# Performance work log

Hardware: AMD Instinct MI355X
Metric: run time of the kernel (lower is better)

Reference implementation:

```python
import jax, jax.numpy as jnp
import numpy as np

N_NODES = 50000
N_EDGES = 800000
D_N = 64      # node feature dim
D_E = 64      # edge feature dim
HID = 128     # MLP hidden dim
D_OUT = 64    # edge/node MLP output dim


def _mlp_params(key, d_in, d_hid, d_out):
    k1, k2 = jax.random.split(key)
    s1 = 1.0 / np.sqrt(d_in)
    s2 = 1.0 / np.sqrt(d_hid)
    return (
        jax.random.uniform(k1, (d_in, d_hid), jnp.float32, -s1, s1),
        jnp.zeros((d_hid,), jnp.float32),
        jax.random.uniform(k2, (d_hid, d_out), jnp.float32, -s2, s2),
        jnp.zeros((d_out,), jnp.float32),
    )


def setup_inputs() -> dict:
    key = jax.random.key(0)
    ks = jax.random.split(key, 7)
    nf = jax.random.normal(ks[0], (N_NODES, D_N), jnp.float32)
    ef = jax.random.normal(ks[1], (N_EDGES, D_E), jnp.float32)
    src = jax.random.randint(ks[2], (N_EDGES,), 0, N_NODES, jnp.int64)
    dst = jax.random.randint(ks[3], (N_EDGES,), 0, N_NODES, jnp.int64)
    We1, be1, We2, be2 = _mlp_params(ks[4], 2 * D_N + D_E, HID, D_OUT)
    Wa1, ba1, Wa2, ba2 = _mlp_params(ks[5], 2 * D_N + D_E, HID, D_OUT)
    Wn1, bn1, Wn2, bn2 = _mlp_params(ks[6], D_OUT + D_N, HID, D_OUT)
    return dict(nf=nf, ef=ef, src=src, dst=dst,
                We1=We1, be1=be1, We2=We2, be2=be2,
                Wa1=Wa1, ba1=ba1, Wa2=Wa2, ba2=ba2,
                Wn1=Wn1, bn1=bn1, Wn2=Wn2, bn2=bn2)


def _mlp(x, W1, b1, W2, b2):
    return jax.nn.relu(x @ W1 + b1) @ W2 + b2


def reference(nf, ef, src, dst,
              We1, be1, We2, be2,
              Wa1, ba1, Wa2, ba2,
              Wn1, bn1, Wn2, bn2):
    # edge update: gather src/dst node feats, concat with edge feats  [E, 2*D_N + D_E]
    x_e = jnp.concatenate([nf[src], nf[dst], ef], axis=-1)
    e_out = _mlp(x_e, We1, be1, We2, be2)                 # [E, D_OUT]
    gate = jax.nn.sigmoid(_mlp(x_e, Wa1, ba1, Wa2, ba2))  # [E, D_OUT]
    updated_ef = gate * e_out                              # message m == updated edge feat
    # scatter-sum messages into destination nodes
    agg_m = jax.ops.segment_sum(updated_ef, dst, num_segments=N_NODES)  # [N, D_OUT]
    # node update
    x_n = jnp.concatenate([agg_m, nf], axis=-1)            # [N, D_OUT + D_N]
    updated_nf = _mlp(x_n, Wn1, bn1, Wn2, bn2)             # [N, D_OUT]
    return updated_nf, updated_ef
```

## Files before the change

kernel.cpp:

```cpp
#include <hip/hip_runtime.h>

#define NN 50000
#define NE 800000

typedef float f32x4 __attribute__((ext_vector_type(4)));
typedef short s16x8 __attribute__((ext_vector_type(8)));
typedef unsigned short u16;

__device__ __forceinline__ u16 f2bf(float f) {
  union { float f; unsigned u; } v; v.f = f;
  unsigned r = v.u + 0x7FFFu + ((v.u >> 16) & 1u);
  return (u16)(r >> 16);
}

__device__ __forceinline__ void st_bf4(u16* p, f32x4 v) {
  ushort4 pv;
  pv.x = f2bf(v.x); pv.y = f2bf(v.y); pv.z = f2bf(v.z); pv.w = f2bf(v.w);
  *(ushort4*)p = pv;
}

__global__ void zero_kernel(f32x4* __restrict__ p) {
  f32x4 z; z[0] = 0.f; z[1] = 0.f; z[2] = 0.f; z[3] = 0.f;
  p[(size_t)blockIdx.x * 256 + threadIdx.x] = z;
}

__device__ __forceinline__ void pack_one(const float* __restrict__ W, int N,
                                         u16* __restrict__ out, int t) {
  int j = t & 7, lane = (t >> 3) & 63, f = t >> 9;
  int NT = N >> 4;
  int nt = f % NT, ks = f / NT;
  int row = ks * 32 + ((lane >> 4) << 3) + j;
  int col = nt * 16 + (lane & 15);
  out[t] = f2bf(W[row * N + col]);
}

__global__ void pack_kernel(const float* __restrict__ We1, const float* __restrict__ We2,
                            const float* __restrict__ Wa1, const float* __restrict__ Wa2,
                            const float* __restrict__ Wn1, const float* __restrict__ Wn2,
                            u16* __restrict__ out) {
  int t = blockIdx.x * 256 + threadIdx.x;
  if (t < 24576)      pack_one(We1, 128, out,          t);
  else if (t < 32768) pack_one(We2, 64,  out + 24576,  t - 24576);
  else if (t < 57344) pack_one(Wa1, 128, out + 32768,  t - 32768);
  else if (t < 65536) pack_one(Wa2, 64,  out + 57344,  t - 57344);
  else if (t < 81920) pack_one(Wn1, 128, out + 65536,  t - 65536);
  else if (t < 90112) pack_one(Wn2, 64,  out + 81920,  t - 81920);
}

__global__ __launch_bounds__(256, 2)
void edge_kernel(const float* __restrict__ nf, const float* __restrict__ ef,
                 const int* __restrict__ src, const int* __restrict__ dst,
                 const u16* __restrict__ W1e, const float* __restrict__ b1e,
                 const u16* __restrict__ W2e, const float* __restrict__ b2e,
                 const u16* __restrict__ W1a, const float* __restrict__ b1a,
                 const u16* __restrict__ W2a, const float* __restrict__ b2a,
                 float* __restrict__ out_ef, float* __restrict__ agg) {
  __shared__ u16 xe[4][16 * 200];
  __shared__ u16 hs[4][16 * 136];
  __shared__ int sdst[4][16];
  const int w = threadIdx.x >> 6, lane = threadIdx.x & 63;
  const int e0 = blockIdx.x * 64 + w * 16;
  const int er = lane >> 4, c4 = (lane & 15) * 4;

  #pragma unroll
  for (int g = 0; g < 4; ++g) {
    int el = g * 4 + er;
    int e = e0 + el;
    int s = src[e], d = dst[e];
    if (c4 == 0) sdst[w][el] = d;
    f32x4 fs = *(const f32x4*)(nf + (size_t)s * 64 + c4);
    f32x4 fd = *(const f32x4*)(nf + (size_t)d * 64 + c4);
    f32x4 fe = *(const f32x4*)(ef + (size_t)e * 64 + c4);
    u16* row = &xe[w][el * 200];
    st_bf4(row + c4, fs);
    st_bf4(row + 64 + c4, fd);
    st_bf4(row + 128 + c4, fe);
  }
  __syncthreads();

  const int m = lane & 15, q = lane >> 4;
  s16x8 a1[6];
  #pragma unroll
  for (int k = 0; k < 6; ++k)
    a1[k] = *(const s16x8*)&xe[w][m * 200 + k * 32 + q * 8];

  f32x4 acc[8];
  #pragma unroll
  for (int i = 0; i < 8; ++i) { acc[i][0] = 0.f; acc[i][1] = 0.f; acc[i][2] = 0.f; acc[i][3] = 0.f; }
  #pragma unroll
  for (int nt = 0; nt < 8; ++nt)
    #pragma unroll
    for (int k = 0; k < 6; ++k) {
      s16x8 b = *(const s16x8*)(W1e + ((size_t)(k * 8 + nt) * 64 + lane) * 8);
      acc[nt] = __builtin_amdgcn_mfma_f32_16x16x32_bf16(a1[k], b, acc[nt], 0, 0, 0);
    }
  #pragma unroll
  for (int nt = 0; nt < 8; ++nt) {
    float bv = b1e[nt * 16 + m];
    #pragma unroll
    for (int r = 0; r < 4; ++r) {
      float h = acc[nt][r] + bv;
      h = h > 0.f ? h : 0.f;
      hs[w][(q * 4 + r) * 136 + nt * 16 + m] = f2bf(h);
    }
  }
  __syncthreads();

  s16x8 a2[4];
  #pragma unroll
  for (int k = 0; k < 4; ++k)
    a2[k] = *(const s16x8*)&hs[w][m * 136 + k * 32 + q * 8];
  f32x4 eo[4];
  #pragma unroll
  for (int i = 0; i < 4; ++i) { eo[i][0] = 0.f; eo[i][1] = 0.f; eo[i][2] = 0.f; eo[i][3] = 0.f; }
  #pragma unroll
  for (int nt = 0; nt < 4; ++nt)
    #pragma unroll
    for (int k = 0; k < 4; ++k) {
      s16x8 b = *(const s16x8*)(W2e + ((size_t)(k * 4 + nt) * 64 + lane) * 8);
      eo[nt] = __builtin_amdgcn_mfma_f32_16x16x32_bf16(a2[k], b, eo[nt], 0, 0, 0);
    }

  f32x4 accg[8];
  #pragma unroll
  for (int i = 0; i < 8; ++i) { accg[i][0] = 0.f; accg[i][1] = 0.f; accg[i][2] = 0.f; accg[i][3] = 0.f; }
  #pragma unroll
  for (int nt = 0; nt < 8; ++nt)
    #pragma unroll
    for (int k = 0; k < 6; ++k) {
      s16x8 b = *(const s16x8*)(W1a + ((size_t)(k * 8 + nt) * 64 + lane) * 8);
      accg[nt] = __builtin_amdgcn_mfma_f32_16x16x32_bf16(a1[k], b, accg[nt], 0, 0, 0);
    }
  __syncthreads();
  #pragma unroll
  for (int nt = 0; nt < 8; ++nt) {
    float bv = b1a[nt * 16 + m];
    #pragma unroll
    for (int r = 0; r < 4; ++r) {
      float h = accg[nt][r] + bv;
      h = h > 0.f ? h : 0.f;
      hs[w][(q * 4 + r) * 136 + nt * 16 + m] = f2bf(h);
    }
  }
  __syncthreads();

  s16x8 a2g[4];
  #pragma unroll
  for (int k = 0; k < 4; ++k)
    a2g[k] = *(const s16x8*)&hs[w][m * 136 + k * 32 + q * 8];
  f32x4 go[4];
  #pragma unroll
  for (int i = 0; i < 4; ++i) { go[i][0] = 0.f; go[i][1] = 0.f; go[i][2] = 0.f; go[i][3] = 0.f; }
  #pragma unroll
  for (int nt = 0; nt < 4; ++nt)
    #pragma unroll
    for (int k = 0; k < 4; ++k) {
      s16x8 b = *(const s16x8*)(W2a + ((size_t)(k * 4 + nt) * 64 + lane) * 8);
      go[nt] = __builtin_amdgcn_mfma_f32_16x16x32_bf16(a2g[k], b, go[nt], 0, 0, 0);
    }

  #pragma unroll
  for (int nt = 0; nt < 4; ++nt) {
    int col = nt * 16 + m;
    float be2v = b2e[col], ba2v = b2a[col];
    #pragma unroll
    for (int r = 0; r < 4; ++r) {
      int rowi = q * 4 + r;
      int e = e0 + rowi;
      float ev = eo[nt][r] + be2v;
      float gv = go[nt][r] + ba2v;
      float gs = 1.f / (1.f + __expf(-gv));
      float val = gs * ev;
      out_ef[(size_t)e * 64 + col] = val;
      atomicAdd(agg + (size_t)sdst[w][rowi] * 64 + col, val);
    }
  }
}

__global__ __launch_bounds__(256, 2)
void node_kernel(const float* __restrict__ nf, const float* __restrict__ agg,
                 const u16* __restrict__ W1n, const float* __restrict__ b1n,
                 const u16* __restrict__ W2n, const float* __restrict__ b2n,
                 float* __restrict__ out_nf) {
  __shared__ u16 xn[4][16 * 136];
  __shared__ u16 hn[4][16 * 136];
  const int w = threadIdx.x >> 6, lane = threadIdx.x & 63;
  const int n0 = blockIdx.x * 64 + w * 16;
  const int er = lane >> 4, c4 = (lane & 15) * 4;

  #pragma unroll
  for (int g = 0; g < 4; ++g) {
    int nl = g * 4 + er;
    int n = n0 + nl; if (n >= NN) n = NN - 1;
    f32x4 fa = *(const f32x4*)(agg + (size_t)n * 64 + c4);
    f32x4 fn = *(const f32x4*)(nf + (size_t)n * 64 + c4);
    u16* row = &xn[w][nl * 136];
    st_bf4(row + c4, fa);
    st_bf4(row + 64 + c4, fn);
  }
  __syncthreads();

  const int m = lane & 15, q = lane >> 4;
  s16x8 a1[4];
  #pragma unroll
  for (int k = 0; k < 4; ++k)
    a1[k] = *(const s16x8*)&xn[w][m * 136 + k * 32 + q * 8];
  f32x4 acc[8];
  #pragma unroll
  for (int i = 0; i < 8; ++i) { acc[i][0] = 0.f; acc[i][1] = 0.f; acc[i][2] = 0.f; acc[i][3] = 0.f; }
  #pragma unroll
  for (int nt = 0; nt < 8; ++nt)
    #pragma unroll
    for (int k = 0; k < 4; ++k) {
      s16x8 b = *(const s16x8*)(W1n + ((size_t)(k * 8 + nt) * 64 + lane) * 8);
      acc[nt] = __builtin_amdgcn_mfma_f32_16x16x32_bf16(a1[k], b, acc[nt], 0, 0, 0);
    }
  #pragma unroll
  for (int nt = 0; nt < 8; ++nt) {
    float bv = b1n[nt * 16 + m];
    #pragma unroll
    for (int r = 0; r < 4; ++r) {
      float h = acc[nt][r] + bv;
      h = h > 0.f ? h : 0.f;
      hn[w][(q * 4 + r) * 136 + nt * 16 + m] = f2bf(h);
    }
  }
  __syncthreads();

  s16x8 a2[4];
  #pragma unroll
  for (int k = 0; k < 4; ++k)
    a2[k] = *(const s16x8*)&hn[w][m * 136 + k * 32 + q * 8];
  f32x4 o[4];
  #pragma unroll
  for (int i = 0; i < 4; ++i) { o[i][0] = 0.f; o[i][1] = 0.f; o[i][2] = 0.f; o[i][3] = 0.f; }
  #pragma unroll
  for (int nt = 0; nt < 4; ++nt)
    #pragma unroll
    for (int k = 0; k < 4; ++k) {
      s16x8 b = *(const s16x8*)(W2n + ((size_t)(k * 4 + nt) * 64 + lane) * 8);
      o[nt] = __builtin_amdgcn_mfma_f32_16x16x32_bf16(a2[k], b, o[nt], 0, 0, 0);
    }
  #pragma unroll
  for (int nt = 0; nt < 4; ++nt) {
    int col = nt * 16 + m;
    float bv = b2n[col];
    #pragma unroll
    for (int r = 0; r < 4; ++r) {
      int rowi = q * 4 + r;
      int n = n0 + rowi;
      if (n < NN) out_nf[(size_t)n * 64 + col] = o[nt][r] + bv;
    }
  }
}

extern "C" void kernel_launch(void* const* d_in, const int* in_sizes, int n_in,
                              void* d_out, int out_size, void* d_ws, size_t ws_size,
                              hipStream_t stream) {
  const float* nf  = (const float*)d_in[0];
  const float* ef  = (const float*)d_in[1];
  const int*   src = (const int*)d_in[2];
  const int*   dst = (const int*)d_in[3];
  const float* We1 = (const float*)d_in[4];
  const float* be1 = (const float*)d_in[5];
  const float* We2 = (const float*)d_in[6];
  const float* be2 = (const float*)d_in[7];
  const float* Wa1 = (const float*)d_in[8];
  const float* ba1 = (const float*)d_in[9];
  const float* Wa2 = (const float*)d_in[10];
  const float* ba2 = (const float*)d_in[11];
  const float* Wn1 = (const float*)d_in[12];
  const float* bn1 = (const float*)d_in[13];
  const float* Wn2 = (const float*)d_in[14];
  const float* bn2 = (const float*)d_in[15];
  float* out = (float*)d_out;
  float* agg = (float*)d_ws;
  u16* pk = (u16*)((char*)d_ws + (size_t)NN * 64 * 4);

  zero_kernel<<<3125, 256, 0, stream>>>((f32x4*)agg);
  pack_kernel<<<352, 256, 0, stream>>>(We1, We2, Wa1, Wa2, Wn1, Wn2, pk);
  edge_kernel<<<NE / 64, 256, 0, stream>>>(nf, ef, src, dst,
      pk, be1, pk + 24576, be2, pk + 32768, ba1, pk + 57344, ba2,
      out + (size_t)NN * 64, agg);
  node_kernel<<<(NN + 63) / 64, 256, 0, stream>>>(nf, agg,
      pk + 65536, bn1, pk + 81920, bn2, out);
}
```

Before: 719.7 us.

## Replace atomic scatter-add with CSR build and per-node gather reduction

Drops the float atomicAdd scatter into the aggregation buffer. Instead it builds a CSR index by destination node (count, a single-block scan, then scatter of edge ids) and adds a gather kernel that sums each node's messages from the written edge output. The edge kernel also merges its per-wave LDS buffers into one, removes the block-wide syncs because each wave only touches its own region, and raises the occupancy hint to 4. This trades contended float atomics for several extra small kernels, a serial single-block scan, and a random re-read of the 800k×64 message array.

```diff
diff --git a/kernel.cpp b/kernel.cpp
--- a/kernel.cpp
+++ b/kernel.cpp
@@ -17,11 +17,6 @@
   ushort4 pv;
   pv.x = f2bf(v.x); pv.y = f2bf(v.y); pv.z = f2bf(v.z); pv.w = f2bf(v.w);
   *(ushort4*)p = pv;
-}
-
-__global__ void zero_kernel(f32x4* __restrict__ p) {
-  f32x4 z; z[0] = 0.f; z[1] = 0.f; z[2] = 0.f; z[3] = 0.f;
-  p[(size_t)blockIdx.x * 256 + threadIdx.x] = z;
 }
 
 __device__ __forceinline__ void pack_one(const float* __restrict__ W, int N,
@@ -47,42 +42,88 @@
   else if (t < 90112) pack_one(Wn2, 64,  out + 81920,  t - 81920);
 }
 
-__global__ __launch_bounds__(256, 2)
+__global__ void zero_cnt_kernel(int* __restrict__ cnt) {
+  int t = blockIdx.x * 256 + threadIdx.x;
+  if (t < NN) cnt[t] = 0;
+}
+
+__global__ void count_kernel(const int* __restrict__ dst, int* __restrict__ cnt) {
+  int t = blockIdx.x * 256 + threadIdx.x;
+  atomicAdd(cnt + dst[t], 1);
+}
+
+__global__ void scan_kernel(const int* __restrict__ cnt, int* __restrict__ off,
+                            int* __restrict__ head) {
+  __shared__ int s[1024];
+  const int t = threadIdx.x;
+  const int C = 49;
+  const int base = t * C;
+  int sum = 0;
+  for (int i = 0; i < C; ++i) {
+    int idx = base + i;
+    sum += (idx < NN) ? cnt[idx] : 0;
+  }
+  s[t] = sum;
+  __syncthreads();
+  for (int d = 1; d < 1024; d <<= 1) {
+    int v = (t >= d) ? s[t - d] : 0;
+    __syncthreads();
+    s[t] += v;
+    __syncthreads();
+  }
+  int run = (t == 0) ? 0 : s[t - 1];
+  for (int i = 0; i < C; ++i) {
+    int idx = base + i;
+    if (idx < NN) {
+      int c = cnt[idx];
+      off[idx] = run;
+      head[idx] = run;
+      run += c;
+    }
+  }
+  if (t == 1023) off[NN] = run;
+}
+
+__global__ void scatter_kernel(const int* __restrict__ dst, int* __restrict__ head,
+                               int* __restrict__ eidx) {
+  int e = blockIdx.x * 256 + threadIdx.x;
+  int pos = atomicAdd(head + dst[e], 1);
+  eidx[pos] = e;
+}
+
+__global__ __launch_bounds__(256, 4)
 void edge_kernel(const float* __restrict__ nf, const float* __restrict__ ef,
                  const int* __restrict__ src, const int* __restrict__ dst,
                  const u16* __restrict__ W1e, const float* __restrict__ b1e,
                  const u16* __restrict__ W2e, const float* __restrict__ b2e,
                  const u16* __restrict__ W1a, const float* __restrict__ b1a,
                  const u16* __restrict__ W2a, const float* __restrict__ b2a,
-                 float* __restrict__ out_ef, float* __restrict__ agg) {
-  __shared__ u16 xe[4][16 * 200];
-  __shared__ u16 hs[4][16 * 136];
-  __shared__ int sdst[4][16];
+                 float* __restrict__ out_ef) {
+  __shared__ u16 lds[4][3200];
   const int w = threadIdx.x >> 6, lane = threadIdx.x & 63;
   const int e0 = blockIdx.x * 64 + w * 16;
   const int er = lane >> 4, c4 = (lane & 15) * 4;
+  u16* X = lds[w];
 
   #pragma unroll
   for (int g = 0; g < 4; ++g) {
     int el = g * 4 + er;
     int e = e0 + el;
     int s = src[e], d = dst[e];
-    if (c4 == 0) sdst[w][el] = d;
     f32x4 fs = *(const f32x4*)(nf + (size_t)s * 64 + c4);
     f32x4 fd = *(const f32x4*)(nf + (size_t)d * 64 + c4);
     f32x4 fe = *(const f32x4*)(ef + (size_t)e * 64 + c4);
-    u16* row = &xe[w][el * 200];
+    u16* row = X + el * 200;
     st_bf4(row + c4, fs);
     st_bf4(row + 64 + c4, fd);
     st_bf4(row + 128 + c4, fe);
   }
-  __syncthreads();
 
   const int m = lane & 15, q = lane >> 4;
   s16x8 a1[6];
   #pragma unroll
   for (int k = 0; k < 6; ++k)
-    a1[k] = *(const s16x8*)&xe[w][m * 200 + k * 32 + q * 8];
+    a1[k] = *(const s16x8*)&X[m * 200 + k * 32 + q * 8];
 
   f32x4 acc[8];
   #pragma unroll
@@ -101,15 +142,14 @@
     for (int r = 0; r < 4; ++r) {
       float h = acc[nt][r] + bv;
       h = h > 0.f ? h : 0.f;
-      hs[w][(q * 4 + r) * 136 + nt * 16 + m] = f2bf(h);
-    }
-  }
-  __syncthreads();
+      X[(q * 4 + r) * 136 + nt * 16 + m] = f2bf(h);
+    }
+  }
 
   s16x8 a2[4];
   #pragma unroll
   for (int k = 0; k < 4; ++k)
-    a2[k] = *(const s16x8*)&hs[w][m * 136 + k * 32 + q * 8];
+    a2[k] = *(const s16x8*)&X[m * 136 + k * 32 + q * 8];
   f32x4 eo[4];
   #pragma unroll
   for (int i = 0; i < 4; ++i) { eo[i][0] = 0.f; eo[i][1] = 0.f; eo[i][2] = 0.f; eo[i][3] = 0.f; }
@@ -131,7 +171,6 @@
       s16x8 b = *(const s16x8*)(W1a + ((size_t)(k * 8 + nt) * 64 + lane) * 8);
       accg[nt] = __builtin_amdgcn_mfma_f32_16x16x32_bf16(a1[k], b, accg[nt], 0, 0, 0);
     }
-  __syncthreads();
   #pragma unroll
   for (int nt = 0; nt < 8; ++nt) {
     float bv = b1a[nt * 16 + m];
@@ -139,15 +178,14 @@
     for (int r = 0; r < 4; ++r) {
       float h = accg[nt][r] + bv;
       h = h > 0.f ? h : 0.f;
-      hs[w][(q * 4 + r) * 136 + nt * 16 + m] = f2bf(h);
-    }
-  }
-  __syncthreads();
+      X[(q * 4 + r) * 136 + nt * 16 + m] = f2bf(h);
+    }
+  }
 
   s16x8 a2g[4];
   #pragma unroll
   for (int k = 0; k < 4; ++k)
-    a2g[k] = *(const s16x8*)&hs[w][m * 136 + k * 32 + q * 8];
+    a2g[k] = *(const s16x8*)&X[m * 136 + k * 32 + q * 8];
   f32x4 go[4];
   #pragma unroll
   for (int i = 0; i < 4; ++i) { go[i][0] = 0.f; go[i][1] = 0.f; go[i][2] = 0.f; go[i][3] = 0.f; }
@@ -165,16 +203,32 @@
     float be2v = b2e[col], ba2v = b2a[col];
     #pragma unroll
     for (int r = 0; r < 4; ++r) {
-      int rowi = q * 4 + r;
-      int e = e0 + rowi;
+      int e = e0 + q * 4 + r;
       float ev = eo[nt][r] + be2v;
       float gv = go[nt][r] + ba2v;
       float gs = 1.f / (1.f + __expf(-gv));
-      float val = gs * ev;
-      out_ef[(size_t)e * 64 + col] = val;
-      atomicAdd(agg + (size_t)sdst[w][rowi] * 64 + col, val);
-    }
-  }
+      out_ef[(size_t)e * 64 + col] = gs * ev;
+    }
+  }
+}
+
+__global__ __launch_bounds__(256, 4)
+void gather_kernel(const float* __restrict__ msg, const int* __restrict__ off,
+                   const int* __restrict__ eidx, float* __restrict__ agg) {
+  const int w = threadIdx.x >> 6, lane = threadIdx.x & 63;
+  const int n = blockIdx.x * 4 + w;
+  const int s0 = off[n], s1 = off[n + 1];
+  float acc = 0.f;
+  int i = s0;
+  for (; i + 1 < s1; i += 2) {
+    int e0 = eidx[i], e1 = eidx[i + 1];
+    float v0 = msg[(size_t)e0 * 64 + lane];
+    float v1 = msg[(size_t)e1 * 64 + lane];
+    acc += v0;
+    acc += v1;
+  }
+  if (i < s1) acc += msg[(size_t)eidx[i] * 64 + lane];
+  agg[(size_t)n * 64 + lane] = acc;
 }
 
 __global__ __launch_bounds__(256, 2)
@@ -247,8 +301,7 @@
     float bv = b2n[col];
     #pragma unroll
     for (int r = 0; r < 4; ++r) {
-      int rowi = q * 4 + r;
-      int n = n0 + rowi;
+      int n = n0 + q * 4 + r;
       if (n < NN) out_nf[(size_t)n * 64 + col] = o[nt][r] + bv;
     }
   }
@@ -274,14 +327,24 @@
   const float* Wn2 = (const float*)d_in[14];
   const float* bn2 = (const float*)d_in[15];
   float* out = (float*)d_out;
-  float* agg = (float*)d_ws;
-  u16* pk = (u16*)((char*)d_ws + (size_t)NN * 64 * 4);
-
-  zero_kernel<<<3125, 256, 0, stream>>>((f32x4*)agg);
+  float* out_ef = out + (size_t)NN * 64;
+
+  char* w0 = (char*)d_ws;
+  float* agg = (float*)w0;
+  u16*   pk  = (u16*)(w0 + 12800000);
+  int*   cnt = (int*)(w0 + 12980480);
+  int*   off = (int*)(w0 + 13180480);
+  int*   head= (int*)(w0 + 13380544);
+  int*   eidx= (int*)(w0 + 13580544);
+
   pack_kernel<<<352, 256, 0, stream>>>(We1, We2, Wa1, Wa2, Wn1, Wn2, pk);
+  zero_cnt_kernel<<<196, 256, 0, stream>>>(cnt);
+  count_kernel<<<3125, 256, 0, stream>>>(dst, cnt);
+  scan_kernel<<<1, 1024, 0, stream>>>(cnt, off, head);
+  scatter_kernel<<<3125, 256, 0, stream>>>(dst, head, eidx);
   edge_kernel<<<NE / 64, 256, 0, stream>>>(nf, ef, src, dst,
-      pk, be1, pk + 24576, be2, pk + 32768, ba1, pk + 57344, ba2,
-      out + (size_t)NN * 64, agg);
+      pk, be1, pk + 24576, be2, pk + 32768, ba1, pk + 57344, ba2, out_ef);
+  gather_kernel<<<NN / 4, 256, 0, stream>>>(out_ef, off, eidx, agg);
   node_kernel<<<(NN + 63) / 64, 256, 0, stream>>>(nf, agg,
       pk + 65536, bn1, pk + 81920, bn2, out);
 }
```

Measured after the change: 981.6 us. 1.36x slower.
